# Optimization experiments

Hardware: AMD Instinct MI355X
Metric: run time of the kernel (lower is better)

Reference implementation:

```python
import jax, jax.numpy as jnp
import numpy as np

N_BATCH = 128   # C: number of PWL channels / generator batch
N_PTS = 32768   # N: samples per channel
K_PWL = 20      # breakpoints per piecewise-linear function
LATENT = 8
HID = 8
EPS = 1e-7


def _mlp(z, W1, b1, W2, b2):
    # torch mlp: Linear -> Tanh -> Linear -> Tanh
    h = jnp.tanh(z @ W1 + b1)
    return jnp.tanh(h @ W2 + b2)


def _normalize01(a):
    # per-row min/max normalization, a: [C, N]
    a = a - a.min(axis=1, keepdims=True)
    return a / a.max(axis=1, keepdims=True)


def _calibrate1d(x, xp, yp):
    # x: [N, C], xp/yp: [C, K]
    N, C = x.shape
    K = xp.shape[1]
    bp = jnp.concatenate([x[:, :, None], jnp.broadcast_to(xp[None], (N, C, K))], axis=2)  # [N,C,K+1]
    order = jnp.argsort(bp, axis=2)                       # [N,C,K+1]
    sorted_bp = jnp.take_along_axis(bp, order, axis=2)
    x_idx = jnp.argmin(order, axis=2)                     # rank of x among breakpoints
    cand = x_idx - 1
    start_idx = jnp.where(x_idx == 0, 1, jnp.where(x_idx == K, K - 2, cand))
    end_idx = jnp.where(start_idx == cand, start_idx + 2, start_idx + 1)
    start_x = jnp.take_along_axis(sorted_bp, start_idx[..., None], axis=2)[..., 0]
    end_x = jnp.take_along_axis(sorted_bp, end_idx[..., None], axis=2)[..., 0]
    start_idx2 = jnp.where(x_idx == 0, 0, jnp.where(x_idx == K, K - 2, cand))
    yp_e = jnp.broadcast_to(yp[None], (N, C, K))
    start_y = jnp.take_along_axis(yp_e, start_idx2[..., None], axis=2)[..., 0]
    end_y = jnp.take_along_axis(yp_e, (start_idx2 + 1)[..., None], axis=2)[..., 0]
    return start_y + (x - start_x) * (end_y - start_y) / (end_x - start_x + EPS)


def setup_inputs() -> dict:
    key = jax.random.key(0)
    ks = jax.random.split(key, 16)
    s = 0.5
    f32 = jnp.float32
    return {
        "zf": jax.random.normal(ks[0], (N_BATCH, LATENT), f32),
        "zx": jax.random.normal(ks[1], (N_BATCH, N_PTS, LATENT), f32),
        "ze": jax.random.normal(ks[2], (N_BATCH, N_PTS, LATENT), f32),
        "Wx1": jax.random.normal(ks[3], (LATENT, HID), f32) * s,
        "bx1": jax.random.normal(ks[4], (HID,), f32) * s,
        "Wx2": jax.random.normal(ks[5], (HID, 1), f32) * s,
        "bx2": jax.random.normal(ks[6], (1,), f32) * s,
        "We1": jax.random.normal(ks[7], (LATENT, HID), f32) * s,
        "be1": jax.random.normal(ks[8], (HID,), f32) * s,
        "We2": jax.random.normal(ks[9], (HID, 1), f32) * s,
        "be2": jax.random.normal(ks[10], (1,), f32) * s,
        "Wf1": jax.random.normal(ks[11], (LATENT, HID), f32) * s,
        "bf1": jax.random.normal(ks[12], (HID,), f32) * s,
        "Wf2": jax.random.normal(ks[13], (HID, K_PWL), f32) * s,
        "bf2": jax.random.normal(ks[14], (K_PWL,), f32) * s,
        "directions": jax.random.randint(ks[15], (N_BATCH,), 0, 2) > 0,
    }


def reference(zf, zx, ze, Wx1, bx1, Wx2, bx2, We1, be1, We2, be2, Wf1, bf1, Wf2, bf2, directions):
    # gen_f: random ascending/descending monotone PWL per channel
    pts = _mlp(zf, Wf1, bf1, Wf2, bf2)                        # [C, K]
    asc = jnp.sort(pts, axis=1)
    yp = jnp.where(directions[:, None], asc, asc[:, ::-1])    # [C, K]
    xp = jnp.broadcast_to(jnp.linspace(0.0, 1.0, K_PWL, dtype=pts.dtype)[None, :], yp.shape)
    # forward_x: cause variable, per-channel normalized to [0,1]
    x = _mlp(zx, Wx1, bx1, Wx2, bx2)[..., 0]                  # [C, N]
    x = _normalize01(x).T                                     # [N, C]
    # forward_e: standardized noise (global mean / unbiased std)
    e = _mlp(ze, We1, be1, We2, be2)[..., 0].T                # [N, C]
    e = (e - e.mean()) / e.std(ddof=1)
    # forward_y
    y = _calibrate1d(x, xp, yp) + 0.1 * e                     # [N, C]
    return y
```

## Files before the change

### kernel.cpp

```cpp
#include <hip/hip_runtime.h>

#define C_CH  128
#define NP    32768
#define K_PWL 20
#define LAT   8
#define HID   8
#define PTS   4
#define QBLK  (NP / (256 * PTS))

__device__ __forceinline__ float fast_tanh(float x) {
    float e = __expf(2.0f * x);
    return fmaf(-2.0f, __builtin_amdgcn_rcpf(e + 1.0f), 1.0f);
}

__global__ __launch_bounds__(256)
void pass1tile(const float* __restrict__ zx, const float* __restrict__ ze,
               const float* __restrict__ Wx1, const float* __restrict__ bx1,
               const float* __restrict__ Wx2, const float* __restrict__ bx2,
               const float* __restrict__ We1, const float* __restrict__ be1,
               const float* __restrict__ We2, const float* __restrict__ be2,
               float* __restrict__ xtile, float* __restrict__ etile,
               float* __restrict__ pminB, float* __restrict__ pmaxB,
               double* __restrict__ psum) {
    __shared__ float sw[162];
    int t = threadIdx.x;
    if (t < 64)       sw[t] = Wx1[t];
    else if (t < 72)  sw[t] = bx1[t - 64];
    else if (t < 80)  sw[t] = Wx2[t - 72];
    else if (t == 80) sw[80] = bx2[0];
    else if (t < 145) sw[t] = We1[t - 81];
    else if (t < 153) sw[t] = be1[t - 145];
    else if (t < 161) sw[t] = We2[t - 153];
    else if (t == 161) sw[161] = be2[0];
    __syncthreads();

    int c = blockIdx.y;
    int n0 = blockIdx.x * (256 * PTS) + t;
    size_t row = (size_t)c * NP;
    const float4* zx4 = (const float4*)(zx + row * LAT);
    const float4* ze4 = (const float4*)(ze + row * LAT);

    float4 ax[PTS][2], ae[PTS][2];
    #pragma unroll
    for (int k = 0; k < PTS; k++) {
        int n = n0 + k * 256;
        ax[k][0] = zx4[2 * n];  ax[k][1] = zx4[2 * n + 1];
        ae[k][0] = ze4[2 * n];  ae[k][1] = ze4[2 * n + 1];
    }

    float xv[PTS], ev[PTS];
    #pragma unroll
    for (int k = 0; k < PTS; k++) {
        float acc = sw[80];
        #pragma unroll
        for (int j = 0; j < HID; j++) {
            float hh = sw[64 + j];
            hh = fmaf(ax[k][0].x, sw[0 * 8 + j], hh);
            hh = fmaf(ax[k][0].y, sw[1 * 8 + j], hh);
            hh = fmaf(ax[k][0].z, sw[2 * 8 + j], hh);
            hh = fmaf(ax[k][0].w, sw[3 * 8 + j], hh);
            hh = fmaf(ax[k][1].x, sw[4 * 8 + j], hh);
            hh = fmaf(ax[k][1].y, sw[5 * 8 + j], hh);
            hh = fmaf(ax[k][1].z, sw[6 * 8 + j], hh);
            hh = fmaf(ax[k][1].w, sw[7 * 8 + j], hh);
            acc = fmaf(fast_tanh(hh), sw[72 + j], acc);
        }
        xv[k] = fast_tanh(acc);
    }
    #pragma unroll
    for (int k = 0; k < PTS; k++) {
        float acc = sw[161];
        #pragma unroll
        for (int j = 0; j < HID; j++) {
            float hh = sw[145 + j];
            hh = fmaf(ae[k][0].x, sw[81 + 0 * 8 + j], hh);
            hh = fmaf(ae[k][0].y, sw[81 + 1 * 8 + j], hh);
            hh = fmaf(ae[k][0].z, sw[81 + 2 * 8 + j], hh);
            hh = fmaf(ae[k][0].w, sw[81 + 3 * 8 + j], hh);
            hh = fmaf(ae[k][1].x, sw[81 + 4 * 8 + j], hh);
            hh = fmaf(ae[k][1].y, sw[81 + 5 * 8 + j], hh);
            hh = fmaf(ae[k][1].z, sw[81 + 6 * 8 + j], hh);
            hh = fmaf(ae[k][1].w, sw[81 + 7 * 8 + j], hh);
            acc = fmaf(fast_tanh(hh), sw[153 + j], acc);
        }
        ev[k] = fast_tanh(acc);
    }

    float mn = xv[0], mx = xv[0], s = 0.f, s2 = 0.f;
    int cbase = c * 32;
    #pragma unroll
    for (int k = 0; k < PTS; k++) {
        int n = n0 + k * 256;
        int addr = (n >> 5) * (C_CH * 32) + cbase + (n & 31);
        xtile[addr] = xv[k];
        etile[addr] = ev[k];
        mn = fminf(mn, xv[k]); mx = fmaxf(mx, xv[k]);
        s += ev[k]; s2 += ev[k] * ev[k];
    }

    #pragma unroll
    for (int o = 32; o > 0; o >>= 1) {
        mn = fminf(mn, __shfl_down(mn, o));
        mx = fmaxf(mx, __shfl_down(mx, o));
        s += __shfl_down(s, o);
        s2 += __shfl_down(s2, o);
    }
    __shared__ float rmn[4], rmx[4], rs[4], rs2[4];
    int wave = t >> 6, lane = t & 63;
    if (lane == 0) { rmn[wave] = mn; rmx[wave] = mx; rs[wave] = s; rs2[wave] = s2; }
    __syncthreads();
    if (t == 0) {
        for (int w = 1; w < 4; w++) {
            mn = fminf(mn, rmn[w]); mx = fmaxf(mx, rmx[w]);
        }
        int slot = c * QBLK + blockIdx.x;
        pminB[slot] = mn;
        pmaxB[slot] = mx;
        psum[2 * slot]     = (double)rs[0] + (double)rs[1] + (double)rs[2] + (double)rs[3];
        psum[2 * slot + 1] = (double)rs2[0] + (double)rs2[1] + (double)rs2[2] + (double)rs2[3];
    }
}

__global__ __launch_bounds__(256)
void pass2t(const float* __restrict__ xtile, const float* __restrict__ etile,
            const float* __restrict__ zf,
            const float* __restrict__ Wf1, const float* __restrict__ bf1,
            const float* __restrict__ Wf2, const float* __restrict__ bf2,
            const unsigned char* __restrict__ dirs_raw,
            const float* __restrict__ pminB, const float* __restrict__ pmaxB,
            const double* __restrict__ psum,
            float* __restrict__ out) {
    __shared__ float ytile[C_CH * 33];
    __shared__ float syp[C_CH * K_PWL];
    __shared__ float smin[C_CH], sinv[C_CH];
    __shared__ double sred[8];
    __shared__ float sstat[2];
    __shared__ int is_i32;

    int t = threadIdx.x;
    int wave = t >> 6, lane = t & 63;

    if (t == 0) {
        const int* di = (const int*)dirs_raw;
        int ok = 1;
        for (int i = 0; i < 32; i++) { int v = di[i]; if (v != 0 && v != 1) ok = 0; }
        is_i32 = ok;
    }
    __syncthreads();

    if (t >= C_CH) {
        int cc = t - C_CH;
        float z[LAT];
        #pragma unroll
        for (int l = 0; l < LAT; l++) z[l] = zf[cc * LAT + l];
        float h[HID];
        #pragma unroll
        for (int j = 0; j < HID; j++) {
            float a = bf1[j];
            #pragma unroll
            for (int l = 0; l < LAT; l++) a = fmaf(z[l], Wf1[l * HID + j], a);
            h[j] = fast_tanh(a);
        }
        float p[K_PWL];
        #pragma unroll
        for (int k = 0; k < K_PWL; k++) {
            float a = bf2[k];
            #pragma unroll
            for (int j = 0; j < HID; j++) a = fmaf(h[j], Wf2[j * K_PWL + k], a);
            p[k] = fast_tanh(a);
        }
        #pragma unroll
        for (int ph = 0; ph < K_PWL; ph++) {
            #pragma unroll
            for (int k = (ph & 1); k + 1 < K_PWL; k += 2) {
                float lo = fminf(p[k], p[k + 1]);
                float hi = fmaxf(p[k], p[k + 1]);
                p[k] = lo; p[k + 1] = hi;
            }
        }
        int dir = is_i32 ? (((const int*)dirs_raw)[cc] != 0) : (dirs_raw[cc] != 0);
        #pragma unroll
        for (int k = 0; k < K_PWL; k++)
            syp[cc * K_PWL + k] = dir ? p[k] : p[K_PWL - 1 - k];
    } else {
        float mn = 3.0e38f, mx = -3.0e38f;
        int base = t * QBLK;
        #pragma unroll 8
        for (int qq = 0; qq < QBLK; ++qq) {
            mn = fminf(mn, pminB[base + qq]);
            mx = fmaxf(mx, pmaxB[base + qq]);
        }
        smin[t] = mn;
        sinv[t] = __builtin_amdgcn_rcpf(mx - mn);
    }

    double S = 0.0, S2 = 0.0;
    for (int i = t; i < C_CH * QBLK; i += 256) {
        S  += psum[2 * i];
        S2 += psum[2 * i + 1];
    }
    #pragma unroll
    for (int o = 32; o > 0; o >>= 1) {
        S  += __shfl_down(S, o);
        S2 += __shfl_down(S2, o);
    }
    if (lane == 0) { sred[wave] = S; sred[4 + wave] = S2; }
    __syncthreads();
    if (t == 0) {
        S  = sred[0] + sred[1] + sred[2] + sred[3];
        S2 = sred[4] + sred[5] + sred[6] + sred[7];
        double M = (double)C_CH * NP;
        double mean = S / M;
        double var = (S2 - S * S / M) / (M - 1.0);
        sstat[0] = (float)mean;
        sstat[1] = (float)(0.1 / sqrt(var));
    }
    __syncthreads();

    const float INV_DENOM = 1.0f / (1.0f / 19.0f + 1e-7f);
    float mean = sstat[0], escale = sstat[1];
    size_t tbase = (size_t)blockIdx.x * (C_CH * 32);
    int n0 = blockIdx.x * 32;

    const float4* xt4 = (const float4*)(xtile + tbase);
    const float4* et4 = (const float4*)(etile + tbase);
    #pragma unroll
    for (int i = 0; i < 4; i++) {
        int i4 = i * 256 + t;
        float4 xq = xt4[i4];
        float4 eq = et4[i4];
        int c = i4 >> 3;
        int j0 = (i4 & 7) * 4;
        float sm = smin[c], si = sinv[c];
        int sb = c * K_PWL;
        int yb = c * 33 + j0;
        {
            float xn = (xq.x - sm) * si;
            int seg = (int)floorf(xn * 19.0f); seg = max(0, min(18, seg));
            float y0 = syp[sb + seg], y1 = syp[sb + seg + 1];
            float y = fmaf((xn - (float)seg * (1.0f / 19.0f)) * INV_DENOM, y1 - y0, y0);
            ytile[yb + 0] = fmaf(eq.x - mean, escale, y);
        }
        {
            float xn = (xq.y - sm) * si;
            int seg = (int)floorf(xn * 19.0f); seg = max(0, min(18, seg));
            float y0 = syp[sb + seg], y1 = syp[sb + seg + 1];
            float y = fmaf((xn - (float)seg * (1.0f / 19.0f)) * INV_DENOM, y1 - y0, y0);
            ytile[yb + 1] = fmaf(eq.y - mean, escale, y);
        }
        {
            float xn = (xq.z - sm) * si;
            int seg = (int)floorf(xn * 19.0f); seg = max(0, min(18, seg));
            float y0 = syp[sb + seg], y1 = syp[sb + seg + 1];
            float y = fmaf((xn - (float)seg * (1.0f / 19.0f)) * INV_DENOM, y1 - y0, y0);
            ytile[yb + 2] = fmaf(eq.z - mean, escale, y);
        }
        {
            float xn = (xq.w - sm) * si;
            int seg = (int)floorf(xn * 19.0f); seg = max(0, min(18, seg));
            float y0 = syp[sb + seg], y1 = syp[sb + seg + 1];
            float y = fmaf((xn - (float)seg * (1.0f / 19.0f)) * INV_DENOM, y1 - y0, y0);
            ytile[yb + 3] = fmaf(eq.w - mean, escale, y);
        }
    }
    __syncthreads();
    #pragma unroll
    for (int i = 0; i < 16; i++) {
        int idx = i * 256 + t;
        int j = idx >> 7;
        int c = idx & 127;
        out[(size_t)(n0 + j) * C_CH + c] = ytile[c * 33 + j];
    }
}

extern "C" void kernel_launch(void* const* d_in, const int* in_sizes, int n_in,
                              void* d_out, int out_size, void* d_ws, size_t ws_size,
                              hipStream_t stream) {
    const float* zf  = (const float*)d_in[0];
    const float* zx  = (const float*)d_in[1];
    const float* ze  = (const float*)d_in[2];
    const float* Wx1 = (const float*)d_in[3];
    const float* bx1 = (const float*)d_in[4];
    const float* Wx2 = (const float*)d_in[5];
    const float* bx2 = (const float*)d_in[6];
    const float* We1 = (const float*)d_in[7];
    const float* be1 = (const float*)d_in[8];
    const float* We2 = (const float*)d_in[9];
    const float* be2 = (const float*)d_in[10];
    const float* Wf1 = (const float*)d_in[11];
    const float* bf1 = (const float*)d_in[12];
    const float* Wf2 = (const float*)d_in[13];
    const float* bf2 = (const float*)d_in[14];
    const unsigned char* dirs = (const unsigned char*)d_in[15];

    double* psum  = (double*)d_ws;
    float*  pminB = (float*)(psum + 2 * C_CH * QBLK);
    float*  pmaxB = pminB + C_CH * QBLK;
    float*  xtile = pmaxB + C_CH * QBLK;
    float*  etile = xtile + (size_t)C_CH * NP;

    hipLaunchKernelGGL(pass1tile, dim3(QBLK, C_CH), dim3(256), 0, stream,
                       zx, ze, Wx1, bx1, Wx2, bx2, We1, be1, We2, be2,
                       xtile, etile, pminB, pmaxB, psum);
    hipLaunchKernelGGL(pass2t, dim3(NP / 32), dim3(256), 0, stream,
                       xtile, etile, zf, Wf1, bf1, Wf2, bf2, dirs,
                       pminB, pmaxB, psum, (float*)d_out);
}
```

Baseline: 334.7 us.

## Fuse both passes into one persistent cooperative kernel with grid sync

```diff
diff --git a/kernel.cpp b/kernel.cpp
--- a/kernel.cpp
+++ b/kernel.cpp
@@ -1,4 +1,7 @@
 #include <hip/hip_runtime.h>
+#include <hip/hip_cooperative_groups.h>
+
+namespace cg = cooperative_groups;
 
 #define C_CH  128
 #define NP    32768
@@ -7,10 +10,283 @@
 #define HID   8
 #define PTS   4
 #define QBLK  (NP / (256 * PTS))
+#define NITEMS (C_CH * QBLK)
+#define NTILES (NP / 32)
 
 __device__ __forceinline__ float fast_tanh(float x) {
     float e = __expf(2.0f * x);
     return fmaf(-2.0f, __builtin_amdgcn_rcpf(e + 1.0f), 1.0f);
+}
+
+__global__ __launch_bounds__(256, 2)
+void fused3(const float* __restrict__ zf, const float* __restrict__ zx,
+            const float* __restrict__ ze,
+            const float* __restrict__ Wx1, const float* __restrict__ bx1,
+            const float* __restrict__ Wx2, const float* __restrict__ bx2,
+            const float* __restrict__ We1, const float* __restrict__ be1,
+            const float* __restrict__ We2, const float* __restrict__ be2,
+            const float* __restrict__ Wf1, const float* __restrict__ bf1,
+            const float* __restrict__ Wf2, const float* __restrict__ bf2,
+            const unsigned char* __restrict__ dirs_raw,
+            float* __restrict__ out,
+            float* __restrict__ xtile, float* __restrict__ etile,
+            float* __restrict__ pminB, float* __restrict__ pmaxB,
+            double* __restrict__ psum,
+            int nblk) {
+    __shared__ float sw[162];
+    __shared__ float ytile[C_CH * 33];
+    __shared__ float syp[C_CH * K_PWL];
+    __shared__ float smin[C_CH], sinv[C_CH];
+    __shared__ float rmn[4], rmx[4], rs[4], rs2[4];
+    __shared__ double sred[8];
+    __shared__ float sstat[2];
+    __shared__ int is_i32;
+
+    int t = threadIdx.x;
+    int wave = t >> 6, lane = t & 63;
+
+    if (t < 64)       sw[t] = Wx1[t];
+    else if (t < 72)  sw[t] = bx1[t - 64];
+    else if (t < 80)  sw[t] = Wx2[t - 72];
+    else if (t == 80) sw[80] = bx2[0];
+    else if (t < 145) sw[t] = We1[t - 81];
+    else if (t < 153) sw[t] = be1[t - 145];
+    else if (t < 161) sw[t] = We2[t - 153];
+    else if (t == 161) sw[161] = be2[0];
+    __syncthreads();
+
+    int wpb = NITEMS / nblk;
+    for (int wi = 0; wi < wpb; ++wi) {
+        int item = blockIdx.x * wpb + wi;
+        int c = item >> 5;
+        int q = item & (QBLK - 1);
+        int n0 = q * (256 * PTS) + t;
+        size_t row = (size_t)c * NP;
+        const float4* zx4 = (const float4*)(zx + row * LAT);
+        const float4* ze4 = (const float4*)(ze + row * LAT);
+
+        float4 ax[PTS][2], ae[PTS][2];
+        #pragma unroll
+        for (int k = 0; k < PTS; k++) {
+            int n = n0 + k * 256;
+            ax[k][0] = zx4[2 * n];  ax[k][1] = zx4[2 * n + 1];
+            ae[k][0] = ze4[2 * n];  ae[k][1] = ze4[2 * n + 1];
+        }
+
+        float xv[PTS], ev[PTS];
+        #pragma unroll
+        for (int k = 0; k < PTS; k++) {
+            float acc = sw[80];
+            #pragma unroll
+            for (int j = 0; j < HID; j++) {
+                float hh = sw[64 + j];
+                hh = fmaf(ax[k][0].x, sw[0 * 8 + j], hh);
+                hh = fmaf(ax[k][0].y, sw[1 * 8 + j], hh);
+                hh = fmaf(ax[k][0].z, sw[2 * 8 + j], hh);
+                hh = fmaf(ax[k][0].w, sw[3 * 8 + j], hh);
+                hh = fmaf(ax[k][1].x, sw[4 * 8 + j], hh);
+                hh = fmaf(ax[k][1].y, sw[5 * 8 + j], hh);
+                hh = fmaf(ax[k][1].z, sw[6 * 8 + j], hh);
+                hh = fmaf(ax[k][1].w, sw[7 * 8 + j], hh);
+                acc = fmaf(fast_tanh(hh), sw[72 + j], acc);
+            }
+            xv[k] = fast_tanh(acc);
+        }
+        #pragma unroll
+        for (int k = 0; k < PTS; k++) {
+            float acc = sw[161];
+            #pragma unroll
+            for (int j = 0; j < HID; j++) {
+                float hh = sw[145 + j];
+                hh = fmaf(ae[k][0].x, sw[81 + 0 * 8 + j], hh);
+                hh = fmaf(ae[k][0].y, sw[81 + 1 * 8 + j], hh);
+                hh = fmaf(ae[k][0].z, sw[81 + 2 * 8 + j], hh);
+                hh = fmaf(ae[k][0].w, sw[81 + 3 * 8 + j], hh);
+                hh = fmaf(ae[k][1].x, sw[81 + 4 * 8 + j], hh);
+                hh = fmaf(ae[k][1].y, sw[81 + 5 * 8 + j], hh);
+                hh = fmaf(ae[k][1].z, sw[81 + 6 * 8 + j], hh);
+                hh = fmaf(ae[k][1].w, sw[81 + 7 * 8 + j], hh);
+                acc = fmaf(fast_tanh(hh), sw[153 + j], acc);
+            }
+            ev[k] = fast_tanh(acc);
+        }
+
+        float mn = xv[0], mx = xv[0], s = 0.f, s2 = 0.f;
+        int cbase = c * 32;
+        #pragma unroll
+        for (int k = 0; k < PTS; k++) {
+            int n = n0 + k * 256;
+            int addr = (n >> 5) * (C_CH * 32) + cbase + (n & 31);
+            xtile[addr] = xv[k];
+            etile[addr] = ev[k];
+            mn = fminf(mn, xv[k]); mx = fmaxf(mx, xv[k]);
+            s += ev[k]; s2 += ev[k] * ev[k];
+        }
+
+        #pragma unroll
+        for (int o = 32; o > 0; o >>= 1) {
+            mn = fminf(mn, __shfl_down(mn, o));
+            mx = fmaxf(mx, __shfl_down(mx, o));
+            s += __shfl_down(s, o);
+            s2 += __shfl_down(s2, o);
+        }
+        if (lane == 0) { rmn[wave] = mn; rmx[wave] = mx; rs[wave] = s; rs2[wave] = s2; }
+        __syncthreads();
+        if (t == 0) {
+            for (int w = 1; w < 4; w++) {
+                mn = fminf(mn, rmn[w]); mx = fmaxf(mx, rmx[w]);
+            }
+            pminB[item] = mn;
+            pmaxB[item] = mx;
+            psum[2 * item]     = (double)rs[0] + (double)rs[1] + (double)rs[2] + (double)rs[3];
+            psum[2 * item + 1] = (double)rs2[0] + (double)rs2[1] + (double)rs2[2] + (double)rs2[3];
+        }
+        __syncthreads();
+    }
+
+    __threadfence();
+    cg::this_grid().sync();
+
+    if (t == 0) {
+        const int* di = (const int*)dirs_raw;
+        int ok = 1;
+        for (int i = 0; i < 32; i++) { int v = di[i]; if (v != 0 && v != 1) ok = 0; }
+        is_i32 = ok;
+    }
+    __syncthreads();
+
+    if (t >= C_CH) {
+        int cc = t - C_CH;
+        float z[LAT];
+        #pragma unroll
+        for (int l = 0; l < LAT; l++) z[l] = zf[cc * LAT + l];
+        float h[HID];
+        #pragma unroll
+        for (int j = 0; j < HID; j++) {
+            float a = bf1[j];
+            #pragma unroll
+            for (int l = 0; l < LAT; l++) a = fmaf(z[l], Wf1[l * HID + j], a);
+            h[j] = fast_tanh(a);
+        }
+        float p[K_PWL];
+        #pragma unroll
+        for (int k = 0; k < K_PWL; k++) {
+            float a = bf2[k];
+            #pragma unroll
+            for (int j = 0; j < HID; j++) a = fmaf(h[j], Wf2[j * K_PWL + k], a);
+            p[k] = fast_tanh(a);
+        }
+        #pragma unroll
+        for (int ph = 0; ph < K_PWL; ph++) {
+            #pragma unroll
+            for (int k = (ph & 1); k + 1 < K_PWL; k += 2) {
+                float lo = fminf(p[k], p[k + 1]);
+                float hi = fmaxf(p[k], p[k + 1]);
+                p[k] = lo; p[k + 1] = hi;
+            }
+        }
+        int dir = is_i32 ? (((const int*)dirs_raw)[cc] != 0) : (dirs_raw[cc] != 0);
+        #pragma unroll
+        for (int k = 0; k < K_PWL; k++)
+            syp[cc * K_PWL + k] = dir ? p[k] : p[K_PWL - 1 - k];
+    } else {
+        const volatile float* vmin = pminB;
+        const volatile float* vmax = pmaxB;
+        float mn = 3.0e38f, mx = -3.0e38f;
+        int base = t * QBLK;
+        #pragma unroll 8
+        for (int qq = 0; qq < QBLK; ++qq) {
+            mn = fminf(mn, vmin[base + qq]);
+            mx = fmaxf(mx, vmax[base + qq]);
+        }
+        smin[t] = mn;
+        sinv[t] = __builtin_amdgcn_rcpf(mx - mn);
+    }
+
+    {
+        const volatile double* vs = psum;
+        double S = 0.0, S2 = 0.0;
+        for (int i = t; i < NITEMS; i += 256) {
+            S  += vs[2 * i];
+            S2 += vs[2 * i + 1];
+        }
+        #pragma unroll
+        for (int o = 32; o > 0; o >>= 1) {
+            S  += __shfl_down(S, o);
+            S2 += __shfl_down(S2, o);
+        }
+        if (lane == 0) { sred[wave] = S; sred[4 + wave] = S2; }
+    }
+    __syncthreads();
+    if (t == 0) {
+        double S  = sred[0] + sred[1] + sred[2] + sred[3];
+        double S2 = sred[4] + sred[5] + sred[6] + sred[7];
+        double M = (double)C_CH * NP;
+        double mean = S / M;
+        double var = (S2 - S * S / M) / (M - 1.0);
+        sstat[0] = (float)mean;
+        sstat[1] = (float)(0.1 / sqrt(var));
+    }
+    __syncthreads();
+
+    const float INV_DENOM = 1.0f / (1.0f / 19.0f + 1e-7f);
+    float mean = sstat[0], escale = sstat[1];
+    int tpb = NTILES / nblk;
+
+    for (int T = blockIdx.x * tpb; T < blockIdx.x * tpb + tpb; ++T) {
+        size_t tbase = (size_t)T * (C_CH * 32);
+        int n0 = T * 32;
+        const float4* xt4 = (const float4*)(xtile + tbase);
+        const float4* et4 = (const float4*)(etile + tbase);
+        #pragma unroll
+        for (int i = 0; i < 4; i++) {
+            int i4 = i * 256 + t;
+            float4 xq = xt4[i4];
+            float4 eq = et4[i4];
+            int c = i4 >> 3;
+            int j0 = (i4 & 7) * 4;
+            float sm = smin[c], si = sinv[c];
+            int sb = c * K_PWL;
+            int yb = c * 33 + j0;
+            {
+                float xn = (xq.x - sm) * si;
+                int seg = (int)floorf(xn * 19.0f); seg = max(0, min(18, seg));
+                float y0 = syp[sb + seg], y1 = syp[sb + seg + 1];
+                float y = fmaf((xn - (float)seg * (1.0f / 19.0f)) * INV_DENOM, y1 - y0, y0);
+                ytile[yb + 0] = fmaf(eq.x - mean, escale, y);
+            }
+            {
+                float xn = (xq.y - sm) * si;
+                int seg = (int)floorf(xn * 19.0f); seg = max(0, min(18, seg));
+                float y0 = syp[sb + seg], y1 = syp[sb + seg + 1];
+                float y = fmaf((xn - (float)seg * (1.0f / 19.0f)) * INV_DENOM, y1 - y0, y0);
+                ytile[yb + 1] = fmaf(eq.y - mean, escale, y);
+            }
+            {
+                float xn = (xq.z - sm) * si;
+                int seg = (int)floorf(xn * 19.0f); seg = max(0, min(18, seg));
+                float y0 = syp[sb + seg], y1 = syp[sb + seg + 1];
+                float y = fmaf((xn - (float)seg * (1.0f / 19.0f)) * INV_DENOM, y1 - y0, y0);
+                ytile[yb + 2] = fmaf(eq.z - mean, escale, y);
+            }
+            {
+                float xn = (xq.w - sm) * si;
+                int seg = (int)floorf(xn * 19.0f); seg = max(0, min(18, seg));
+                float y0 = syp[sb + seg], y1 = syp[sb + seg + 1];
+                float y = fmaf((xn - (float)seg * (1.0f / 19.0f)) * INV_DENOM, y1 - y0, y0);
+                ytile[yb + 3] = fmaf(eq.w - mean, escale, y);
+            }
+        }
+        __syncthreads();
+        #pragma unroll
+        for (int i = 0; i < 16; i++) {
+            int idx = i * 256 + t;
+            int j = idx >> 7;
+            int c = idx & 127;
+            out[(size_t)(n0 + j) * C_CH + c] = ytile[c * 33 + j];
+        }
+        __syncthreads();
+    }
 }
 
 __global__ __launch_bounds__(256)
@@ -195,7 +471,7 @@
     }
 
     double S = 0.0, S2 = 0.0;
-    for (int i = t; i < C_CH * QBLK; i += 256) {
+    for (int i = t; i < NITEMS; i += 256) {
         S  += psum[2 * i];
         S2 += psum[2 * i + 1];
     }
@@ -292,17 +568,53 @@
     const float* Wf2 = (const float*)d_in[13];
     const float* bf2 = (const float*)d_in[14];
     const unsigned char* dirs = (const unsigned char*)d_in[15];
+    float* outp = (float*)d_out;
 
     double* psum  = (double*)d_ws;
-    float*  pminB = (float*)(psum + 2 * C_CH * QBLK);
-    float*  pmaxB = pminB + C_CH * QBLK;
-    float*  xtile = pmaxB + C_CH * QBLK;
+    float*  pminB = (float*)(psum + 2 * NITEMS);
+    float*  pmaxB = pminB + NITEMS;
+    float*  xtile = pmaxB + NITEMS;
     float*  etile = xtile + (size_t)C_CH * NP;
+
+    static int mode = -1;
+    if (mode < 0) {
+        int dev = 0, coop = 0, nb = 0, mpc = 0;
+        hipGetDevice(&dev);
+        hipDeviceGetAttribute(&coop, hipDeviceAttributeCooperativeLaunch, dev);
+        hipDeviceGetAttribute(&mpc, hipDeviceAttributeMultiprocessorCount, dev);
+        hipError_t oe = hipOccupancyMaxActiveBlocksPerMultiprocessor(
+            &nb, reinterpret_cast<const void*>(fused3), 256, 0);
+        mode = 0;
+        if (coop && oe == hipSuccess && mpc > 0) {
+            long cap = (long)nb * mpc;
+            if (cap >= 1024) mode = 1024;
+            else if (cap >= 512) mode = 512;
+        }
+    }
+
+    if (mode >= 512) {
+        int nblk = mode;
+        void* args[] = {
+            (void*)&zf,  (void*)&zx,  (void*)&ze,
+            (void*)&Wx1, (void*)&bx1, (void*)&Wx2, (void*)&bx2,
+            (void*)&We1, (void*)&be1, (void*)&We2, (void*)&be2,
+            (void*)&Wf1, (void*)&bf1, (void*)&Wf2, (void*)&bf2,
+            (void*)&dirs, (void*)&outp,
+            (void*)&xtile, (void*)&etile,
+            (void*)&pminB, (void*)&pmaxB, (void*)&psum,
+            (void*)&nblk
+        };
+        hipError_t le = hipLaunchCooperativeKernel(
+            reinterpret_cast<const void*>(fused3), dim3(nblk), dim3(256),
+            args, 0, stream);
+        if (le == hipSuccess) return;
+        mode = 0;
+    }
 
     hipLaunchKernelGGL(pass1tile, dim3(QBLK, C_CH), dim3(256), 0, stream,
                        zx, ze, Wx1, bx1, Wx2, bx2, We1, be1, We2, be2,
                        xtile, etile, pminB, pmaxB, psum);
     hipLaunchKernelGGL(pass2t, dim3(NP / 32), dim3(256), 0, stream,
                        xtile, etile, zf, Wf1, bf1, Wf2, bf2, dirs,
-                       pminB, pmaxB, psum, (float*)d_out);
+                       pminB, pmaxB, psum, outp);
 }
```

After: 336.7 us. About the same (+0.6%).
